# Kernel tuning notes

Measured on AMD Instinct MI355X. Metric: run time of the kernel, lower is better.

The kernel has to match this reference:

```python
import jax, jax.numpy as jnp
import numpy as np
import math

H = 16
DQ = 64
NEG = -1000000000.0


def setup_inputs() -> dict:
    key = jax.random.key(0)
    ks = jax.random.split(key, 8)
    B, S, D = 2, 2048, 1024
    scale = 1.0 / math.sqrt(D)
    return {
        "embedding": jax.random.normal(ks[0], (B, S, D), dtype=jnp.float32),
        "mask": jax.random.randint(ks[1], (B, 1, S), 0, 2, dtype=jnp.int32),
        "Wq": jax.random.normal(ks[2], (D, D), dtype=jnp.float32) * scale,
        "bq": jnp.zeros((D,), dtype=jnp.float32),
        "Wk": jax.random.normal(ks[3], (D, D), dtype=jnp.float32) * scale,
        "bk": jnp.zeros((D,), dtype=jnp.float32),
        "Wv": jax.random.normal(ks[4], (D, D), dtype=jnp.float32) * scale,
        "bv": jnp.zeros((D,), dtype=jnp.float32),
        "Wo": jax.random.normal(ks[5], (D, D), dtype=jnp.float32) * scale,
        "bo": jnp.zeros((D,), dtype=jnp.float32),
    }


def reference(embedding, mask, Wq, bq, Wk, bk, Wv, bv, Wo, bo):
    B, S, D = embedding.shape
    # projections -> [B, H, S, DQ]
    def proj(W, b):
        return (embedding @ W + b).reshape(B, S, H, DQ).transpose(0, 2, 1, 3)
    q, k, v = proj(Wq, bq), proj(Wk, bk), proj(Wv, bv)
    scores = jnp.einsum("bhqd,bhkd->bhqk", q, k) / math.sqrt(DQ)
    m = mask[:, None]  # [B,1,1,S] broadcasts over heads and query positions
    scores = jnp.where(m == 0, NEG, scores)
    attn = jax.nn.softmax(scores, axis=-1)
    x = jnp.einsum("bhqk,bhkd->bhqd", attn, v)
    x = x.transpose(0, 2, 1, 3).reshape(B, S, H * DQ)
    return x @ Wo + bo
```

## Files before the change

kernel.cpp:

```cpp
#include <hip/hip_runtime.h>
#include <stdint.h>

#define B_ 2
#define S_ 2048
#define D_ 1024
#define H_ 16
#define DQ_ 64
#define M_ 4096
#define CLOG2 16.0f
#define NEGB -1000000000.0f

typedef unsigned short ushort_t;
typedef __attribute__((ext_vector_type(8))) short short8;
typedef __attribute__((ext_vector_type(4))) float floatx4;
typedef __attribute__((ext_vector_type(16))) float floatx16;

#if __has_builtin(__builtin_amdgcn_exp2f)
#define EXP2(x) __builtin_amdgcn_exp2f(x)
#else
#define EXP2(x) exp2f(x)
#endif

__device__ __forceinline__ ushort_t f2bf(float f) {
  union { float f; uint32_t u; } v; v.f = f;
  uint32_t r = v.u + 0x7FFFu + ((v.u >> 16) & 1u);
  return (ushort_t)(r >> 16);
}

__device__ __forceinline__ ushort_t f2bf_trunc(float f) {
  union { float f; uint32_t u; } v; v.f = f;
  return (ushort_t)(v.u >> 16);
}

__device__ __forceinline__ void async16(const ushort_t* g, ushort_t* l) {
  __builtin_amdgcn_global_load_lds(
      (const __attribute__((address_space(1))) uint32_t*)g,
      (__attribute__((address_space(3))) uint32_t*)l, 16, 0, 0);
}


__global__ void k_cvt_emb(const float* __restrict__ in, ushort_t* __restrict__ out) {
  int i = (blockIdx.x * 256 + threadIdx.x) * 4;
  float4 v = *(const float4*)(in + i);
  uint64_t pk = (uint64_t)f2bf(v.x) | ((uint64_t)f2bf(v.y) << 16) |
                ((uint64_t)f2bf(v.z) << 32) | ((uint64_t)f2bf(v.w) << 48);
  *(uint64_t*)(out + i) = pk;
}

__global__ void k_cvt_w(const float* __restrict__ Wq, const float* __restrict__ Wk,
                        const float* __restrict__ Wv, const float* __restrict__ Wo,
                        ushort_t* __restrict__ Wt) {
  const float* W = (blockIdx.z == 0) ? Wq : (blockIdx.z == 1) ? Wk
                 : (blockIdx.z == 2) ? Wv : Wo;
  ushort_t* out = Wt + (size_t)blockIdx.z * D_ * D_;
  __shared__ float t[32][33];
  int k0 = blockIdx.x * 32, n0 = blockIdx.y * 32;
  int tx = threadIdx.x, ty = threadIdx.y;
  for (int r = 0; r < 32; r += 8)
    t[ty + r][tx] = W[(size_t)(k0 + ty + r) * D_ + n0 + tx];
  __syncthreads();
  for (int r = 0; r < 32; r += 8)
    out[(size_t)(n0 + ty + r) * D_ + k0 + tx] = f2bf(t[tx][ty + r]);
}

template <int IM>
__device__ __forceinline__ void gemm_core2(const ushort_t* __restrict__ A,
                                           const ushort_t* __restrict__ Bt,
                                           ushort_t* As, ushort_t* Bs,
                                           int m0, int n0, floatx4 (&acc)[IM][4]) {
  int t = threadIdx.x, lane = t & 63, w = t >> 6;
  int wm = (w >> 1) * (IM * 16), wn = (w & 1) * 64;
  int l15 = lane & 15, quad = lane >> 4;
  int srow8 = (lane >> 3) & 7;
  int sch = ((lane & 7) ^ srow8) * 8;
  const ushort_t* Ag = A + (size_t)(m0 + w * 8 + srow8) * D_ + sch;
  const ushort_t* Bg = Bt + (size_t)(n0 + w * 8 + srow8) * D_ + sch;
  for (int kt = 0; kt < D_; kt += 64) {
    __syncthreads();
#pragma unroll
    for (int c = 0; c < IM; c++)
      async16(Ag + kt + (size_t)c * 32 * D_, As + (c * 32 + w * 8) * 64);
#pragma unroll
    for (int c = 0; c < 4; c++)
      async16(Bg + kt + (size_t)c * 32 * D_, Bs + (c * 32 + w * 8) * 64);
    __syncthreads();
#pragma unroll
    for (int ks = 0; ks < 2; ks++) {
      int ch = ((ks * 4 + quad) ^ (l15 & 7)) * 8;
      short8 a[IM], b[4];
#pragma unroll
      for (int i = 0; i < IM; i++)
        a[i] = *(const short8*)(As + (wm + i * 16 + l15) * 64 + ch);
#pragma unroll
      for (int j = 0; j < 4; j++)
        b[j] = *(const short8*)(Bs + (wn + j * 16 + l15) * 64 + ch);
#pragma unroll
      for (int i = 0; i < IM; i++)
#pragma unroll
        for (int j = 0; j < 4; j++)
          acc[i][j] = __builtin_amdgcn_mfma_f32_16x16x32_bf16(a[i], b[j], acc[i][j], 0, 0, 0);
    }
  }
}

__global__ __launch_bounds__(256, 3) void k_proj(
    const ushort_t* __restrict__ A, const ushort_t* __restrict__ Wt,
    const float* __restrict__ bq, const float* __restrict__ bk,
    const float* __restrict__ bv,
    ushort_t* __restrict__ Q, ushort_t* __restrict__ K, ushort_t* __restrict__ V) {
  __shared__ __align__(16) ushort_t As[128 * 64];
  __shared__ __align__(16) ushort_t Bs[128 * 64];
  int z = blockIdx.z;
  const ushort_t* Bt = Wt + (size_t)z * D_ * D_;
  const float* bias = (z == 0) ? bq : (z == 1) ? bk : bv;
  int m0 = blockIdx.x * 128, n0 = blockIdx.y * 128;
  floatx4 acc[4][4] = {};
  gemm_core2<4>(A, Bt, As, Bs, m0, n0, acc);
  int lane = threadIdx.x & 63, w = threadIdx.x >> 6;
  int wm = (w >> 1) * 64, wn = (w & 1) * 64;
  int quad = lane >> 4, l15 = lane & 15;
  float scale = (z == 0) ? 0.125f * 1.44269504f : 1.0f;
#pragma unroll
  for (int i = 0; i < 4; i++)
#pragma unroll
    for (int j = 0; j < 4; j++) {
      int ncol = n0 + wn + j * 16 + l15;
      float bb = bias[ncol];
      int h = ncol >> 6, dq = ncol & 63;
      int m = m0 + wm + i * 16 + quad * 4;
      int b = m >> 11, s = m & (S_ - 1);
      if (z == 2) {
        uint64_t pk = (uint64_t)f2bf(acc[i][j][0] + bb) |
                      ((uint64_t)f2bf(acc[i][j][1] + bb) << 16) |
                      ((uint64_t)f2bf(acc[i][j][2] + bb) << 32) |
                      ((uint64_t)f2bf(acc[i][j][3] + bb) << 48);
        *(uint64_t*)(V + ((size_t)(b * H_ + h) * DQ_ + dq) * S_ + s) = pk;
      } else {
        ushort_t* dst = (z == 0) ? Q : K;
#pragma unroll
        for (int r = 0; r < 4; r++)
          dst[((size_t)(b * H_ + h) * S_ + (s + r)) * DQ_ + dq] =
              f2bf((acc[i][j][r] + bb) * scale);
      }
    }
}

__global__ __launch_bounds__(256, 2) void k_attn(
    const ushort_t* __restrict__ Q, const ushort_t* __restrict__ Kg,
    const ushort_t* __restrict__ Vt, const int* __restrict__ mask,
    ushort_t* __restrict__ X) {
  int bh = blockIdx.y, b = bh >> 4, h = bh & 15;
  int t = threadIdx.x, lane = t & 63, w = t >> 6;
  int l31 = lane & 31, hi = lane >> 5;
  int q0 = blockIdx.x * 128 + w * 32;
  const ushort_t* Qh = Q + (size_t)bh * S_ * DQ_;
  const ushort_t* Kh = Kg + (size_t)bh * S_ * DQ_;
  const ushort_t* Vh = Vt + (size_t)bh * DQ_ * S_;
  const int* mb = mask + b * S_;

  __shared__ __align__(16) ushort_t Ks[64 * 64];
  __shared__ __align__(16) ushort_t Vs[64 * 64];
  __shared__ __align__(16) ushort_t Ps[4][32 * 72];

  short8 qf[4];
#pragma unroll
  for (int ks = 0; ks < 4; ks++)
    qf[ks] = *(const short8*)(Qh + (size_t)(q0 + l31) * DQ_ + ks * 16 + hi * 8);

  int srow8 = (lane >> 3) & 7;
  int sch = ((lane & 7) ^ srow8) * 8;
  const ushort_t* Kg1 = Kh + (size_t)(w * 8 + srow8) * DQ_ + sch;
  const ushort_t* Vg1 = Vh + (size_t)(w * 8 + srow8) * S_ + sch;

  floatx16 o[2] = {};
  float lp[16] = {};

  for (int k0 = 0; k0 < S_; k0 += 64) {
    __syncthreads();
    async16(Kg1 + (size_t)k0 * DQ_, Ks + w * 512);
    async16(Kg1 + (size_t)(k0 + 32) * DQ_, Ks + w * 512 + 2048);
    async16(Vg1 + k0, Vs + w * 512);
    async16(Vg1 + (size_t)32 * S_ + k0, Vs + w * 512 + 2048);
    __syncthreads();

    floatx16 s0 = {}, s1 = {};
#pragma unroll
    for (int ks = 0; ks < 4; ks++) {
      int ch = ((ks * 2 + hi) ^ (l31 & 7)) * 8;
      short8 kf0 = *(const short8*)(Ks + l31 * 64 + ch);
      short8 kf1 = *(const short8*)(Ks + (32 + l31) * 64 + ch);
      s0 = __builtin_amdgcn_mfma_f32_32x32x16_bf16(qf[ks], kf0, s0, 0, 0, 0);
      s1 = __builtin_amdgcn_mfma_f32_32x32x16_bf16(qf[ks], kf1, s1, 0, 0, 0);
    }

    float b0 = mb[k0 + l31] ? -CLOG2 : NEGB;
    float b1 = mb[k0 + 32 + l31] ? -CLOG2 : NEGB;

    ushort_t* Pw = Ps[w];
#pragma unroll
    for (int r = 0; r < 16; r++) {
      int qrow = (r & 3) + 8 * (r >> 2) + 4 * hi;
      float p0 = EXP2(s0[r] + b0);
      float p1 = EXP2(s1[r] + b1);
      lp[r] += p0 + p1;
      Pw[qrow * 72 + l31] = f2bf_trunc(p0);
      Pw[qrow * 72 + 32 + l31] = f2bf_trunc(p1);
    }

#pragma unroll
    for (int ks = 0; ks < 4; ks++) {
      short8 pf = *(const short8*)(Pw + l31 * 72 + ks * 16 + hi * 8);
      int ch = ((ks * 2 + hi) ^ (l31 & 7)) * 8;
      short8 vf0 = *(const short8*)(Vs + l31 * 64 + ch);
      short8 vf1 = *(const short8*)(Vs + (32 + l31) * 64 + ch);
      o[0] = __builtin_amdgcn_mfma_f32_32x32x16_bf16(pf, vf0, o[0], 0, 0, 0);
      o[1] = __builtin_amdgcn_mfma_f32_32x32x16_bf16(pf, vf1, o[1], 0, 0, 0);
    }
  }

#pragma unroll
  for (int r = 0; r < 16; r++) {
    float l = lp[r];
    for (int d = 1; d < 32; d <<= 1) l += __shfl_xor(l, d, 64);
    float inv = 1.0f / l;
    int qrow = q0 + (r & 3) + 8 * (r >> 2) + 4 * hi;
    size_t base = ((size_t)(b * S_ + qrow)) * D_ + h * DQ_;
    X[base + l31] = f2bf(o[0][r] * inv);
    X[base + 32 + l31] = f2bf(o[1][r] * inv);
  }
}

__global__ __launch_bounds__(256, 2) void k_oproj(
    const ushort_t* __restrict__ A, const ushort_t* __restrict__ Wt,
    const float* __restrict__ bias, float* __restrict__ C) {
  __shared__ __align__(16) ushort_t As[64 * 64];
  __shared__ __align__(16) ushort_t Bs[128 * 64];
  int m0 = blockIdx.x * 64, n0 = blockIdx.y * 128;
  floatx4 acc[2][4] = {};
  gemm_core2<2>(A, Wt, As, Bs, m0, n0, acc);
  int lane = threadIdx.x & 63, w = threadIdx.x >> 6;
  int wm = (w >> 1) * 32, wn = (w & 1) * 64;
  int quad = lane >> 4, l15 = lane & 15;
#pragma unroll
  for (int i = 0; i < 2; i++)
#pragma unroll
    for (int j = 0; j < 4; j++) {
      int ncol = n0 + wn + j * 16 + l15;
      float bb = bias[ncol];
      int mr = m0 + wm + i * 16 + quad * 4;
#pragma unroll
      for (int r = 0; r < 4; r++)
        C[(size_t)(mr + r) * D_ + ncol] = acc[i][j][r] + bb;
    }
}

extern "C" void kernel_launch(void* const* d_in, const int* in_sizes, int n_in,
                              void* d_out, int out_size, void* d_ws, size_t ws_size,
                              hipStream_t stream) {
  const float* emb  = (const float*)d_in[0];
  const int*   mask = (const int*)d_in[1];
  const float* Wq = (const float*)d_in[2];
  const float* bq = (const float*)d_in[3];
  const float* Wk = (const float*)d_in[4];
  const float* bk = (const float*)d_in[5];
  const float* Wv = (const float*)d_in[6];
  const float* bv = (const float*)d_in[7];
  const float* Wo = (const float*)d_in[8];
  const float* bo = (const float*)d_in[9];
  float* out = (float*)d_out;

  ushort_t* embb = (ushort_t*)d_ws;
  ushort_t* Wt   = embb + (size_t)M_ * D_;
  ushort_t* Qb   = Wt + (size_t)4 * D_ * D_;
  ushort_t* Kb   = Qb + (size_t)M_ * D_;
  ushort_t* Vb   = Kb + (size_t)M_ * D_;
  ushort_t* Xb   = Vb + (size_t)M_ * D_;

  k_cvt_emb<<<dim3(M_ * D_ / 1024), 256, 0, stream>>>(emb, embb);
  k_cvt_w<<<dim3(32, 32, 4), dim3(32, 8), 0, stream>>>(Wq, Wk, Wv, Wo, Wt);
  k_proj<<<dim3(32, 8, 3), 256, 0, stream>>>(embb, Wt, bq, bk, bv, Qb, Kb, Vb);
  k_attn<<<dim3(16, 32), 256, 0, stream>>>(Qb, Kb, Vb, mask, Xb);
  k_oproj<<<dim3(64, 8), 256, 0, stream>>>(Xb, Wt + (size_t)3 * D_ * D_, bo, out);
}
```

Before: 201.5 us.

## Keep softmax probabilities in registers via transposed MFMA and bitmask masking

Swaps the MFMA operand order so the score tile comes out transposed. Each lane then holds one query row, and the P tile can be built for the PV MFMA from registers with a single cross-half shuffle instead of going through a shared-memory round trip. The mask is precomputed into 64-bit ballot words by a new small kernel, so masked keys become a zero via a bit test instead of a per-tile int load. The row sum becomes per-lane, which cuts the final 5-step shuffle reduction to one, and output stores are packed into 8-byte writes. The cost is an extra kernel launch and some register shuffling and selects in the inner loop.

```diff
diff --git a/kernel.cpp b/kernel.cpp
--- a/kernel.cpp
+++ b/kernel.cpp
@@ -8,7 +8,6 @@
 #define DQ_ 64
 #define M_ 4096
 #define CLOG2 16.0f
-#define NEGB -1000000000.0f
 
 typedef unsigned short ushort_t;
 typedef __attribute__((ext_vector_type(8))) short short8;
@@ -27,9 +26,12 @@
   return (ushort_t)(r >> 16);
 }
 
-__device__ __forceinline__ ushort_t f2bf_trunc(float f) {
-  union { float f; uint32_t u; } v; v.f = f;
-  return (ushort_t)(v.u >> 16);
+__device__ __forceinline__ uint32_t pk2_trunc(float a, float b) {
+  union { float f; uint32_t u; } va, vb; va.f = a; vb.f = b;
+  return (va.u >> 16) | (vb.u & 0xFFFF0000u);
+}
+__device__ __forceinline__ uint32_t pk2_rne(float a, float b) {
+  return (uint32_t)f2bf(a) | ((uint32_t)f2bf(b) << 16);
 }
 
 __device__ __forceinline__ void async16(const ushort_t* g, ushort_t* l) {
@@ -61,6 +63,12 @@
   __syncthreads();
   for (int r = 0; r < 32; r += 8)
     out[(size_t)(n0 + ty + r) * D_ + k0 + tx] = f2bf(t[tx][ty + r]);
+}
+
+__global__ void k_cvt_mask(const int* __restrict__ mask, uint64_t* __restrict__ mbits) {
+  int b = blockIdx.y, tile = blockIdx.x, lane = threadIdx.x;
+  unsigned long long w = __ballot(mask[b * S_ + tile * 64 + lane] != 0);
+  if (lane == 0) mbits[b * 32 + tile] = w;
 }
 
 template <int IM>
@@ -147,7 +155,7 @@
 
 __global__ __launch_bounds__(256, 2) void k_attn(
     const ushort_t* __restrict__ Q, const ushort_t* __restrict__ Kg,
-    const ushort_t* __restrict__ Vt, const int* __restrict__ mask,
+    const ushort_t* __restrict__ Vt, const uint64_t* __restrict__ mbits,
     ushort_t* __restrict__ X) {
   int bh = blockIdx.y, b = bh >> 4, h = bh & 15;
   int t = threadIdx.x, lane = t & 63, w = t >> 6;
@@ -156,11 +164,10 @@
   const ushort_t* Qh = Q + (size_t)bh * S_ * DQ_;
   const ushort_t* Kh = Kg + (size_t)bh * S_ * DQ_;
   const ushort_t* Vh = Vt + (size_t)bh * DQ_ * S_;
-  const int* mb = mask + b * S_;
+  const uint64_t* mbp = mbits + b * 32;
 
   __shared__ __align__(16) ushort_t Ks[64 * 64];
   __shared__ __align__(16) ushort_t Vs[64 * 64];
-  __shared__ __align__(16) ushort_t Ps[4][32 * 72];
 
   short8 qf[4];
 #pragma unroll
@@ -173,7 +180,7 @@
   const ushort_t* Vg1 = Vh + (size_t)(w * 8 + srow8) * S_ + sch;
 
   floatx16 o[2] = {};
-  float lp[16] = {};
+  float lsum = 0.0f;
 
   for (int k0 = 0; k0 < S_; k0 += 64) {
     __syncthreads();
@@ -189,45 +196,62 @@
       int ch = ((ks * 2 + hi) ^ (l31 & 7)) * 8;
       short8 kf0 = *(const short8*)(Ks + l31 * 64 + ch);
       short8 kf1 = *(const short8*)(Ks + (32 + l31) * 64 + ch);
-      s0 = __builtin_amdgcn_mfma_f32_32x32x16_bf16(qf[ks], kf0, s0, 0, 0, 0);
-      s1 = __builtin_amdgcn_mfma_f32_32x32x16_bf16(qf[ks], kf1, s1, 0, 0, 0);
-    }
-
-    float b0 = mb[k0 + l31] ? -CLOG2 : NEGB;
-    float b1 = mb[k0 + 32 + l31] ? -CLOG2 : NEGB;
-
-    ushort_t* Pw = Ps[w];
-#pragma unroll
-    for (int r = 0; r < 16; r++) {
-      int qrow = (r & 3) + 8 * (r >> 2) + 4 * hi;
-      float p0 = EXP2(s0[r] + b0);
-      float p1 = EXP2(s1[r] + b1);
-      lp[r] += p0 + p1;
-      Pw[qrow * 72 + l31] = f2bf_trunc(p0);
-      Pw[qrow * 72 + 32 + l31] = f2bf_trunc(p1);
+      s0 = __builtin_amdgcn_mfma_f32_32x32x16_bf16(kf0, qf[ks], s0, 0, 0, 0);
+      s1 = __builtin_amdgcn_mfma_f32_32x32x16_bf16(kf1, qf[ks], s1, 0, 0, 0);
+    }
+
+    uint64_t mb64 = mbp[k0 >> 6];
+    uint32_t pk[2][4][2];
+#pragma unroll
+    for (int g = 0; g < 4; g++) {
+      float p0[4], p1[4];
+#pragma unroll
+      for (int j = 0; j < 4; j++) {
+        int r = g * 4 + j;
+        uint64_t sh = mb64 >> (8 * g + j + 4 * hi);
+        p0[j] = (sh & 1) ? EXP2(s0[r] - CLOG2) : 0.0f;
+        p1[j] = ((sh >> 32) & 1) ? EXP2(s1[r] - CLOG2) : 0.0f;
+        lsum += p0[j] + p1[j];
+      }
+      pk[0][g][0] = pk2_trunc(p0[0], p0[1]); pk[0][g][1] = pk2_trunc(p0[2], p0[3]);
+      pk[1][g][0] = pk2_trunc(p1[0], p1[1]); pk[1][g][1] = pk2_trunc(p1[2], p1[3]);
     }
 
 #pragma unroll
     for (int ks = 0; ks < 4; ks++) {
-      short8 pf = *(const short8*)(Pw + l31 * 72 + ks * 16 + hi * 8);
+      int a = ks >> 1, gb = (ks & 1) * 2;
+      uint32_t pass0 = hi ? pk[a][gb][0]     : pk[a][gb + 1][0];
+      uint32_t pass1 = hi ? pk[a][gb][1]     : pk[a][gb + 1][1];
+      uint32_t own0  = hi ? pk[a][gb + 1][0] : pk[a][gb][0];
+      uint32_t own1  = hi ? pk[a][gb + 1][1] : pk[a][gb][1];
+      uint32_t recv0 = __shfl_xor(pass0, 32, 64);
+      uint32_t recv1 = __shfl_xor(pass1, 32, 64);
+      union { uint32_t u[4]; short8 v; } pf;
+      pf.u[0] = hi ? recv0 : own0;
+      pf.u[1] = hi ? recv1 : own1;
+      pf.u[2] = hi ? own0 : recv0;
+      pf.u[3] = hi ? own1 : recv1;
       int ch = ((ks * 2 + hi) ^ (l31 & 7)) * 8;
       short8 vf0 = *(const short8*)(Vs + l31 * 64 + ch);
       short8 vf1 = *(const short8*)(Vs + (32 + l31) * 64 + ch);
-      o[0] = __builtin_amdgcn_mfma_f32_32x32x16_bf16(pf, vf0, o[0], 0, 0, 0);
-      o[1] = __builtin_amdgcn_mfma_f32_32x32x16_bf16(pf, vf1, o[1], 0, 0, 0);
+      o[0] = __builtin_amdgcn_mfma_f32_32x32x16_bf16(vf0, pf.v, o[0], 0, 0, 0);
+      o[1] = __builtin_amdgcn_mfma_f32_32x32x16_bf16(vf1, pf.v, o[1], 0, 0, 0);
     }
   }
 
-#pragma unroll
-  for (int r = 0; r < 16; r++) {
-    float l = lp[r];
-    for (int d = 1; d < 32; d <<= 1) l += __shfl_xor(l, d, 64);
-    float inv = 1.0f / l;
-    int qrow = q0 + (r & 3) + 8 * (r >> 2) + 4 * hi;
-    size_t base = ((size_t)(b * S_ + qrow)) * D_ + h * DQ_;
-    X[base + l31] = f2bf(o[0][r] * inv);
-    X[base + 32 + l31] = f2bf(o[1][r] * inv);
-  }
+  float l = lsum + __shfl_xor(lsum, 32, 64);
+  float inv = 1.0f / l;
+  int q = q0 + l31;
+  size_t base = (size_t)(b * S_ + q) * D_ + h * DQ_;
+#pragma unroll
+  for (int a = 0; a < 2; a++)
+#pragma unroll
+    for (int g = 0; g < 4; g++) {
+      uint2 st;
+      st.x = pk2_rne(o[a][4 * g] * inv, o[a][4 * g + 1] * inv);
+      st.y = pk2_rne(o[a][4 * g + 2] * inv, o[a][4 * g + 3] * inv);
+      *(uint2*)(X + base + a * 32 + g * 8 + 4 * hi) = st;
+    }
 }
 
 __global__ __launch_bounds__(256, 2) void k_oproj(
@@ -275,10 +299,12 @@
   ushort_t* Kb   = Qb + (size_t)M_ * D_;
   ushort_t* Vb   = Kb + (size_t)M_ * D_;
   ushort_t* Xb   = Vb + (size_t)M_ * D_;
+  uint64_t* Mb   = (uint64_t*)(Xb + (size_t)M_ * D_);
 
   k_cvt_emb<<<dim3(M_ * D_ / 1024), 256, 0, stream>>>(emb, embb);
   k_cvt_w<<<dim3(32, 32, 4), dim3(32, 8), 0, stream>>>(Wq, Wk, Wv, Wo, Wt);
+  k_cvt_mask<<<dim3(32, 2), 64, 0, stream>>>(mask, Mb);
   k_proj<<<dim3(32, 8, 3), 256, 0, stream>>>(embb, Wt, bq, bk, bv, Qb, Kb, Vb);
-  k_attn<<<dim3(16, 32), 256, 0, stream>>>(Qb, Kb, Vb, mask, Xb);
+  k_attn<<<dim3(16, 32), 256, 0, stream>>>(Qb, Kb, Vb, Mb, Xb);
   k_oproj<<<dim3(64, 8), 256, 0, stream>>>(Xb, Wt + (size_t)3 * D_ * D_, bo, out);
 }
```

After: 205.6 us. +2.0%, slower.
